# Kernel tuning notes

Measured on AMD Instinct MI355X. Metric: run time of the kernel, lower is better.

The kernel has to match this reference:

```python
import jax, jax.numpy as jnp
import numpy as np

W_PAD = 1  # reflection pad / stencil half-width
CLAMP_MIN = 0.071
EPS = 1e-05


def _laplacian_kernel():
    k = 2 * W_PAD + 1
    ker = -jnp.ones((1, 1, k, k, k), dtype=jnp.float32)
    ker = ker.at[0, 0, W_PAD, W_PAD, W_PAD].set(float(k * k * k - 1))
    return ker  # [O=1, I=1, 3, 3, 3]


def _boundary_weight(pred):
    # pred: [B, L, D, H, W] raw logits
    B, L, D, H, Wd = pred.shape
    ps = jax.nn.softmax(pred, axis=1).astype(jnp.float32)
    # reflect-pad spatial dims by 1, then clamp (matches torch: pad then clamp)
    p = jnp.pad(ps, ((0, 0), (0, 0), (1, 1), (1, 1), (1, 1)), mode='reflect')
    p = jnp.clip(p, CLAMP_MIN)
    # single-channel 3x3x3 stencil applied independently per (batch, label)
    x = p.reshape(B * L, 1, D + 2, H + 2, Wd + 2)
    bt = jax.lax.conv_general_dilated(
        x, _laplacian_kernel(), window_strides=(1, 1, 1), padding='VALID',
        dimension_numbers=('NCDHW', 'OIDHW', 'NCDHW'))
    bt = jnp.abs(bt).reshape(B, L, D, H, Wd)
    bt = jax.lax.stop_gradient(bt)  # torch .detach()
    return 0.5 / (bt + 0.5)


def _dice_bpm(y_pred, y_true, bpm):
    vol_axes = tuple(range(2, y_pred.ndim))  # spatial dims
    top = 2.0 * jnp.sum(y_true * y_pred * bpm, axis=vol_axes)
    bottom = jnp.clip(jnp.sum((y_true + y_pred) * bpm, axis=vol_axes), EPS)
    return -jnp.mean(top / bottom)


def setup_inputs() -> dict:
    key = jax.random.key(0)
    k1, k2 = jax.random.split(key)
    shape = (2, 8, 128, 128, 128)
    pred = jax.random.normal(k1, shape, dtype=jnp.float32)
    target = jax.random.uniform(k2, shape, dtype=jnp.float32)
    return {"pred": pred, "target": target}


def reference(pred, target):
    focal_weight = _boundary_weight(pred)
    return _dice_bpm(pred, target, focal_weight)
```

## Files before the change

### kernel.cpp

```cpp
#include <hip/hip_runtime.h>

constexpr int Dd = 128, Hh = 128, Ww = 128;
constexpr int B_ = 2, L_ = 8;
constexpr int S_SP = Dd * Hh * Ww;
constexpr float CLAMP_MIN = 0.071f;
constexpr float EPS = 1e-5f;

constexpr int TIL = 16;
constexpr int HALO = TIL + 2;
constexpr int DCH = 16;
constexpr int NPOS = HALO * HALO;
constexpr int BLK_PER_B = (Dd / DCH) * (Hh / TIL) * (Ww / TIL);
constexpr int NBLK = B_ * BLK_PER_B;

__device__ __forceinline__ int refl(int x, int n) {
  return x < 0 ? 1 : (x >= n ? n - 2 : x);
}

__global__ __launch_bounds__(256) void fused_kernel(
    const float* __restrict__ pred, const float* __restrict__ tgt,
    float* __restrict__ partial) {
  __shared__ float sps[NPOS][L_];
  __shared__ float red[4][16];

  int blk = blockIdx.x;
  int tw = blk & 7, th = (blk >> 3) & 7, dc = (blk >> 6) & 7, b = blk >> 9;
  int h0 = th * TIL, w0 = tw * TIL, d0 = dc * DCH;
  int tid = threadIdx.x;
  int hl = tid >> 4, wl = tid & 15;
  const float* predb = pred + (size_t)b * L_ * S_SP;

  float s2m[L_], s2c[L_], s2n[L_], ctrc[L_], ctrn[L_];
  float atop[L_], abot[L_];
#pragma unroll
  for (int l = 0; l < L_; ++l) { atop[l] = 0.f; abot[l] = 0.f; }

  for (int pp = -1; pp <= DCH; ++pp) {
    int pd = d0 + pp;
    int rpd = pd < 0 ? 1 : (pd >= Dd ? Dd - 2 : pd);
    __syncthreads();
    for (int pos = tid; pos < NPOS; pos += 256) {
      int i = pos / HALO, j = pos - i * HALO;
      int gh = refl(h0 - 1 + i, Hh);
      int gw = refl(w0 - 1 + j, Ww);
      const float* src = predb + (size_t)rpd * Hh * Ww + gh * Ww + gw;
      float v[L_];
      float m = -1e30f;
#pragma unroll
      for (int l = 0; l < L_; ++l) { v[l] = src[(size_t)l * S_SP]; m = fmaxf(m, v[l]); }
      float s = 0.f;
#pragma unroll
      for (int l = 0; l < L_; ++l) { v[l] = __expf(v[l] - m); s += v[l]; }
      float inv = 1.f / s;
#pragma unroll
      for (int l = 0; l < L_; ++l) v[l] = fmaxf(v[l] * inv, CLAMP_MIN);
      float4* dst = (float4*)&sps[pos][0];
      dst[0] = make_float4(v[0], v[1], v[2], v[3]);
      dst[1] = make_float4(v[4], v[5], v[6], v[7]);
    }
    __syncthreads();
#pragma unroll
    for (int l = 0; l < L_; ++l) s2n[l] = 0.f;
#pragma unroll
    for (int di = 0; di < 3; ++di) {
#pragma unroll
      for (int dj = 0; dj < 3; ++dj) {
        const float4* q = (const float4*)&sps[(hl + di) * HALO + (wl + dj)][0];
        float4 a = q[0], c4 = q[1];
        s2n[0] += a.x;  s2n[1] += a.y;  s2n[2] += a.z;  s2n[3] += a.w;
        s2n[4] += c4.x; s2n[5] += c4.y; s2n[6] += c4.z; s2n[7] += c4.w;
        if (di == 1 && dj == 1) {
          ctrn[0] = a.x;  ctrn[1] = a.y;  ctrn[2] = a.z;  ctrn[3] = a.w;
          ctrn[4] = c4.x; ctrn[5] = c4.y; ctrn[6] = c4.z; ctrn[7] = c4.w;
        }
      }
    }
    if (pp >= 1) {
      int d = pd - 1;
      size_t off0 = (size_t)b * L_ * S_SP + (size_t)d * Hh * Ww + (h0 + hl) * Ww + (w0 + wl);
#pragma unroll
      for (int l = 0; l < L_; ++l) {
        float sum27 = s2m[l] + s2c[l] + s2n[l];
        float bt = fabsf(27.f * ctrc[l] - sum27);
        float bw = 0.5f / (bt + 0.5f);
        size_t off = off0 + (size_t)l * S_SP;
        float p = pred[off];
        float t = tgt[off];
        atop[l] += t * p * bw;
        abot[l] += (t + p) * bw;
      }
    }
#pragma unroll
    for (int l = 0; l < L_; ++l) { s2m[l] = s2c[l]; s2c[l] = s2n[l]; ctrc[l] = ctrn[l]; }
  }

#pragma unroll
  for (int l = 0; l < L_; ++l) {
#pragma unroll
    for (int o = 32; o > 0; o >>= 1) {
      atop[l] += __shfl_down(atop[l], o, 64);
      abot[l] += __shfl_down(abot[l], o, 64);
    }
  }
  int lane = tid & 63, wv = tid >> 6;
  if (lane == 0) {
#pragma unroll
    for (int l = 0; l < L_; ++l) { red[wv][l * 2] = atop[l]; red[wv][l * 2 + 1] = abot[l]; }
  }
  __syncthreads();
  if (tid < 16) {
    float v = red[0][tid] + red[1][tid] + red[2][tid] + red[3][tid];
    partial[blk * 16 + tid] = v;
  }
}

__global__ void finalize_kernel(const float* __restrict__ partial, float* __restrict__ out) {
  __shared__ float rr[16];
  int t = threadIdx.x;
  int p = t >> 4, k = t & 15;
  int b = p >> 3, l = p & 7;
  float top = 0.f, bot = 0.f;
  for (int m = 0; m < BLK_PER_B / 16; ++m) {
    int blk = b * BLK_PER_B + k * (BLK_PER_B / 16) + m;
    top += partial[blk * 16 + l * 2];
    bot += partial[blk * 16 + l * 2 + 1];
  }
#pragma unroll
  for (int o = 8; o > 0; o >>= 1) {
    top += __shfl_down(top, o, 16);
    bot += __shfl_down(bot, o, 16);
  }
  if (k == 0) rr[p] = 2.f * top / fmaxf(bot, EPS);
  __syncthreads();
  if (t == 0) {
    float s = 0.f;
#pragma unroll
    for (int i = 0; i < 16; ++i) s += rr[i];
    out[0] = -s / 16.f;
  }
}

extern "C" void kernel_launch(void* const* d_in, const int* in_sizes, int n_in,
                              void* d_out, int out_size, void* d_ws, size_t ws_size,
                              hipStream_t stream) {
  const float* pred = (const float*)d_in[0];
  const float* tgt  = (const float*)d_in[1];
  float* partial = (float*)d_ws;

  fused_kernel<<<NBLK, 256, 0, stream>>>(pred, tgt, partial);
  finalize_kernel<<<1, 256, 0, stream>>>(partial, (float*)d_out);
}
```

Baseline: 345.6 us.

## Prefetch next depth slice's halo into registers and halve depth chunk

Loads the next depth plane's halo logits into registers while the current plane is processed through softmax and stencil, so global loads overlap with compute and LDS work. The depth chunk per block drops from 16 to 8, doubling the block count for more parallelism at the cost of more redundant halo planes (10 loaded per 8 output instead of 18 per 16). Register pressure rises from holding two extra 8-element prefetch buffers.

```diff
diff --git a/kernel.cpp b/kernel.cpp
--- a/kernel.cpp
+++ b/kernel.cpp
@@ -8,13 +8,40 @@
 
 constexpr int TIL = 16;
 constexpr int HALO = TIL + 2;
-constexpr int DCH = 16;
+constexpr int DCH = 8;
 constexpr int NPOS = HALO * HALO;
-constexpr int BLK_PER_B = (Dd / DCH) * (Hh / TIL) * (Ww / TIL);
+constexpr int NDC = Dd / DCH;
+constexpr int BLK_PER_B = NDC * (Hh / TIL) * (Ww / TIL);
 constexpr int NBLK = B_ * BLK_PER_B;
 
 __device__ __forceinline__ int refl(int x, int n) {
   return x < 0 ? 1 : (x >= n ? n - 2 : x);
+}
+
+__device__ __forceinline__ void halo_load(const float* __restrict__ predb,
+                                          int rpd, int h0, int w0, int pos,
+                                          float v[L_]) {
+  int i = pos / HALO, j = pos - i * HALO;
+  int gh = refl(h0 - 1 + i, Hh);
+  int gw = refl(w0 - 1 + j, Ww);
+  const float* src = predb + (size_t)rpd * Hh * Ww + gh * Ww + gw;
+#pragma unroll
+  for (int l = 0; l < L_; ++l) v[l] = src[(size_t)l * S_SP];
+}
+
+__device__ __forceinline__ void softmax_store(float v[L_], float* dst8) {
+  float m = v[0];
+#pragma unroll
+  for (int l = 1; l < L_; ++l) m = fmaxf(m, v[l]);
+  float s = 0.f;
+#pragma unroll
+  for (int l = 0; l < L_; ++l) { v[l] = __expf(v[l] - m); s += v[l]; }
+  float inv = 1.f / s;
+#pragma unroll
+  for (int l = 0; l < L_; ++l) v[l] = fmaxf(v[l] * inv, CLAMP_MIN);
+  float4* dst = (float4*)dst8;
+  dst[0] = make_float4(v[0], v[1], v[2], v[3]);
+  dst[1] = make_float4(v[4], v[5], v[6], v[7]);
 }
 
 __global__ __launch_bounds__(256) void fused_kernel(
@@ -24,39 +51,35 @@
   __shared__ float red[4][16];
 
   int blk = blockIdx.x;
-  int tw = blk & 7, th = (blk >> 3) & 7, dc = (blk >> 6) & 7, b = blk >> 9;
+  int tw = blk & 7, th = (blk >> 3) & 7, dc = (blk >> 6) & 15, b = blk >> 10;
   int h0 = th * TIL, w0 = tw * TIL, d0 = dc * DCH;
   int tid = threadIdx.x;
   int hl = tid >> 4, wl = tid & 15;
   const float* predb = pred + (size_t)b * L_ * S_SP;
+  const bool has2 = (tid + 256) < NPOS;
 
   float s2m[L_], s2c[L_], s2n[L_], ctrc[L_], ctrn[L_];
   float atop[L_], abot[L_];
 #pragma unroll
   for (int l = 0; l < L_; ++l) { atop[l] = 0.f; abot[l] = 0.f; }
 
+  float v0[L_], v1[L_];
+  {
+    int pd = d0 - 1;
+    int rpd = pd < 0 ? 1 : (pd >= Dd ? Dd - 2 : pd);
+    halo_load(predb, rpd, h0, w0, tid, v0);
+    if (has2) halo_load(predb, rpd, h0, w0, tid + 256, v1);
+  }
+
   for (int pp = -1; pp <= DCH; ++pp) {
-    int pd = d0 + pp;
-    int rpd = pd < 0 ? 1 : (pd >= Dd ? Dd - 2 : pd);
     __syncthreads();
-    for (int pos = tid; pos < NPOS; pos += 256) {
-      int i = pos / HALO, j = pos - i * HALO;
-      int gh = refl(h0 - 1 + i, Hh);
-      int gw = refl(w0 - 1 + j, Ww);
-      const float* src = predb + (size_t)rpd * Hh * Ww + gh * Ww + gw;
-      float v[L_];
-      float m = -1e30f;
-#pragma unroll
-      for (int l = 0; l < L_; ++l) { v[l] = src[(size_t)l * S_SP]; m = fmaxf(m, v[l]); }
-      float s = 0.f;
-#pragma unroll
-      for (int l = 0; l < L_; ++l) { v[l] = __expf(v[l] - m); s += v[l]; }
-      float inv = 1.f / s;
-#pragma unroll
-      for (int l = 0; l < L_; ++l) v[l] = fmaxf(v[l] * inv, CLAMP_MIN);
-      float4* dst = (float4*)&sps[pos][0];
-      dst[0] = make_float4(v[0], v[1], v[2], v[3]);
-      dst[1] = make_float4(v[4], v[5], v[6], v[7]);
+    softmax_store(v0, &sps[tid][0]);
+    if (has2) softmax_store(v1, &sps[tid + 256][0]);
+    if (pp + 1 <= DCH) {
+      int pdn = d0 + pp + 1;
+      int rpdn = pdn < 0 ? 1 : (pdn >= Dd ? Dd - 2 : pdn);
+      halo_load(predb, rpdn, h0, w0, tid, v0);
+      if (has2) halo_load(predb, rpdn, h0, w0, tid + 256, v1);
     }
     __syncthreads();
 #pragma unroll
@@ -76,7 +99,7 @@
       }
     }
     if (pp >= 1) {
-      int d = pd - 1;
+      int d = d0 + pp - 1;
       size_t off0 = (size_t)b * L_ * S_SP + (size_t)d * Hh * Ww + (h0 + hl) * Ww + (w0 + wl);
 #pragma unroll
       for (int l = 0; l < L_; ++l) {
```

Measured after the change: 362.0 us. 1.05x slower.

## Split softmax into fp16 intermediate pass and per-label register stencil kernel

Applied to the files above, without the earlier changes.

Replaces the fused kernel, which recomputed softmax on every halo cell into shared memory, with two passes. The first computes the clamped softmax once per voxel and writes it as fp16. The second runs the 3x3x3 stencil per (batch, label) from registers and wave shuffles, with vectorized loads, then accumulates the dice sums. This removes the halo recomputation and shared-memory traffic but adds a global round trip of about 67MB of fp16 writes and reads, plus reduced precision in the boundary weight.

```diff
diff --git a/kernel.cpp b/kernel.cpp
--- a/kernel.cpp
+++ b/kernel.cpp
@@ -1,4 +1,5 @@
 #include <hip/hip_runtime.h>
+#include <hip/hip_fp16.h>
 
 constexpr int Dd = 128, Hh = 128, Ww = 128;
 constexpr int B_ = 2, L_ = 8;
@@ -6,111 +7,129 @@
 constexpr float CLAMP_MIN = 0.071f;
 constexpr float EPS = 1e-5f;
 
-constexpr int TIL = 16;
-constexpr int HALO = TIL + 2;
-constexpr int DCH = 16;
-constexpr int NPOS = HALO * HALO;
-constexpr int BLK_PER_B = (Dd / DCH) * (Hh / TIL) * (Ww / TIL);
-constexpr int NBLK = B_ * BLK_PER_B;
+constexpr int DCH = 8;
+constexpr int NDC = Dd / DCH;
+constexpr int NHG = Hh / 16;
+constexpr int BLK_PER_P = NDC * NHG;
+constexpr int NBLK2 = B_ * L_ * BLK_PER_P;
 
-__device__ __forceinline__ int refl(int x, int n) {
-  return x < 0 ? 1 : (x >= n ? n - 2 : x);
+__global__ __launch_bounds__(256) void softmax_fp16_kernel(
+    const float* __restrict__ pred, __half* __restrict__ ps) {
+  const int S4 = S_SP / 4;
+  int g = blockIdx.x * 256 + threadIdx.x;
+  int b = g / S4;
+  int s4 = g - b * S4;
+  const float4* in = (const float4*)(pred + (size_t)b * L_ * S_SP) + s4;
+  float v[L_][4];
+#pragma unroll
+  for (int l = 0; l < L_; ++l) {
+    float4 t = in[(size_t)l * S4];
+    v[l][0] = t.x; v[l][1] = t.y; v[l][2] = t.z; v[l][3] = t.w;
+  }
+#pragma unroll
+  for (int c = 0; c < 4; ++c) {
+    float m = v[0][c];
+#pragma unroll
+    for (int l = 1; l < L_; ++l) m = fmaxf(m, v[l][c]);
+    float s = 0.f;
+#pragma unroll
+    for (int l = 0; l < L_; ++l) { v[l][c] = __expf(v[l][c] - m); s += v[l][c]; }
+    float inv = 1.f / s;
+#pragma unroll
+    for (int l = 0; l < L_; ++l) v[l][c] = fmaxf(v[l][c] * inv, CLAMP_MIN);
+  }
+#pragma unroll
+  for (int l = 0; l < L_; ++l) {
+    __half2 h0 = __floats2half2_rn(v[l][0], v[l][1]);
+    __half2 h1 = __floats2half2_rn(v[l][2], v[l][3]);
+    uint2 u;
+    u.x = *(unsigned*)&h0;
+    u.y = *(unsigned*)&h1;
+    *(uint2*)(ps + ((size_t)(b * L_ + l)) * S_SP + (size_t)s4 * 4) = u;
+  }
 }
 
-__global__ __launch_bounds__(256) void fused_kernel(
-    const float* __restrict__ pred, const float* __restrict__ tgt,
-    float* __restrict__ partial) {
-  __shared__ float sps[NPOS][L_];
-  __shared__ float red[4][16];
+__global__ __launch_bounds__(256) void stencil_dice_kernel(
+    const __half* __restrict__ ps, const float* __restrict__ pred,
+    const float* __restrict__ tgt, float* __restrict__ partial) {
+  int blk = blockIdx.x;
+  int dc = blk & 15;
+  int hg = (blk >> 4) & 7;
+  int bl = blk >> 7;
+  int tid = threadIdx.x;
+  int wl = tid & 15, hl = tid >> 4;
+  int h = hg * 16 + hl;
+  int w0 = wl * 8;
+  int d0 = dc * DCH;
+  const __half* P = ps + (size_t)bl * S_SP;
+  int hm = (h == 0) ? 1 : h - 1;
+  int hp = (h == Hh - 1) ? Hh - 2 : h + 1;
 
-  int blk = blockIdx.x;
-  int tw = blk & 7, th = (blk >> 3) & 7, dc = (blk >> 6) & 7, b = blk >> 9;
-  int h0 = th * TIL, w0 = tw * TIL, d0 = dc * DCH;
-  int tid = threadIdx.x;
-  int hl = tid >> 4, wl = tid & 15;
-  const float* predb = pred + (size_t)b * L_ * S_SP;
+  float s2m[8], s2c[8], cprev[8];
+  float top = 0.f, bot = 0.f;
 
-  float s2m[L_], s2c[L_], s2n[L_], ctrc[L_], ctrn[L_];
-  float atop[L_], abot[L_];
+  for (int t = d0 - 1; t <= d0 + DCH; ++t) {
+    int rt = t < 0 ? 1 : (t > Dd - 1 ? Dd - 2 : t);
+    const __half* plane = P + (size_t)rt * Hh * Ww;
+    float s2n[8], ctr[8];
 #pragma unroll
-  for (int l = 0; l < L_; ++l) { atop[l] = 0.f; abot[l] = 0.f; }
-
-  for (int pp = -1; pp <= DCH; ++pp) {
-    int pd = d0 + pp;
-    int rpd = pd < 0 ? 1 : (pd >= Dd ? Dd - 2 : pd);
-    __syncthreads();
-    for (int pos = tid; pos < NPOS; pos += 256) {
-      int i = pos / HALO, j = pos - i * HALO;
-      int gh = refl(h0 - 1 + i, Hh);
-      int gw = refl(w0 - 1 + j, Ww);
-      const float* src = predb + (size_t)rpd * Hh * Ww + gh * Ww + gw;
-      float v[L_];
-      float m = -1e30f;
+    for (int w = 0; w < 8; ++w) s2n[w] = 0.f;
+    int rows[3] = {hm, h, hp};
 #pragma unroll
-      for (int l = 0; l < L_; ++l) { v[l] = src[(size_t)l * S_SP]; m = fmaxf(m, v[l]); }
-      float s = 0.f;
+    for (int ri = 0; ri < 3; ++ri) {
+      uint4 u = *(const uint4*)(plane + rows[ri] * Ww + w0);
+      float f[8];
+      __half2 a;
+      a = *(__half2*)&u.x; { float2 q = __half22float2(a); f[0] = q.x; f[1] = q.y; }
+      a = *(__half2*)&u.y; { float2 q = __half22float2(a); f[2] = q.x; f[3] = q.y; }
+      a = *(__half2*)&u.z; { float2 q = __half22float2(a); f[4] = q.x; f[5] = q.y; }
+      a = *(__half2*)&u.w; { float2 q = __half22float2(a); f[6] = q.x; f[7] = q.y; }
+      float lf = __shfl_up(f[7], 1, 64);
+      if (wl == 0) lf = f[1];
+      float rg = __shfl_down(f[0], 1, 64);
+      if (wl == 15) rg = f[6];
+      s2n[0] += lf + f[0] + f[1];
 #pragma unroll
-      for (int l = 0; l < L_; ++l) { v[l] = __expf(v[l] - m); s += v[l]; }
-      float inv = 1.f / s;
+      for (int w = 1; w < 7; ++w) s2n[w] += f[w - 1] + f[w] + f[w + 1];
+      s2n[7] += f[6] + f[7] + rg;
+      if (ri == 1) {
 #pragma unroll
-      for (int l = 0; l < L_; ++l) v[l] = fmaxf(v[l] * inv, CLAMP_MIN);
-      float4* dst = (float4*)&sps[pos][0];
-      dst[0] = make_float4(v[0], v[1], v[2], v[3]);
-      dst[1] = make_float4(v[4], v[5], v[6], v[7]);
-    }
-    __syncthreads();
-#pragma unroll
-    for (int l = 0; l < L_; ++l) s2n[l] = 0.f;
-#pragma unroll
-    for (int di = 0; di < 3; ++di) {
-#pragma unroll
-      for (int dj = 0; dj < 3; ++dj) {
-        const float4* q = (const float4*)&sps[(hl + di) * HALO + (wl + dj)][0];
-        float4 a = q[0], c4 = q[1];
-        s2n[0] += a.x;  s2n[1] += a.y;  s2n[2] += a.z;  s2n[3] += a.w;
-        s2n[4] += c4.x; s2n[5] += c4.y; s2n[6] += c4.z; s2n[7] += c4.w;
-        if (di == 1 && dj == 1) {
-          ctrn[0] = a.x;  ctrn[1] = a.y;  ctrn[2] = a.z;  ctrn[3] = a.w;
-          ctrn[4] = c4.x; ctrn[5] = c4.y; ctrn[6] = c4.z; ctrn[7] = c4.w;
-        }
+        for (int w = 0; w < 8; ++w) ctr[w] = f[w];
       }
     }
-    if (pp >= 1) {
-      int d = pd - 1;
-      size_t off0 = (size_t)b * L_ * S_SP + (size_t)d * Hh * Ww + (h0 + hl) * Ww + (w0 + wl);
+    if (t >= d0 + 1) {
+      int d = t - 1;
+      size_t off = (size_t)bl * S_SP + (size_t)d * Hh * Ww + (size_t)h * Ww + w0;
+      float4 p0 = *(const float4*)(pred + off);
+      float4 p1 = *(const float4*)(pred + off + 4);
+      float4 t0 = *(const float4*)(tgt + off);
+      float4 t1 = *(const float4*)(tgt + off + 4);
+      float pv[8] = {p0.x, p0.y, p0.z, p0.w, p1.x, p1.y, p1.z, p1.w};
+      float tv[8] = {t0.x, t0.y, t0.z, t0.w, t1.x, t1.y, t1.z, t1.w};
 #pragma unroll
-      for (int l = 0; l < L_; ++l) {
-        float sum27 = s2m[l] + s2c[l] + s2n[l];
-        float bt = fabsf(27.f * ctrc[l] - sum27);
+      for (int w = 0; w < 8; ++w) {
+        float bt = fabsf(27.f * cprev[w] - (s2m[w] + s2c[w] + s2n[w]));
         float bw = 0.5f / (bt + 0.5f);
-        size_t off = off0 + (size_t)l * S_SP;
-        float p = pred[off];
-        float t = tgt[off];
-        atop[l] += t * p * bw;
-        abot[l] += (t + p) * bw;
+        top += tv[w] * pv[w] * bw;
+        bot += (tv[w] + pv[w]) * bw;
       }
     }
 #pragma unroll
-    for (int l = 0; l < L_; ++l) { s2m[l] = s2c[l]; s2c[l] = s2n[l]; ctrc[l] = ctrn[l]; }
+    for (int w = 0; w < 8; ++w) { s2m[w] = s2c[w]; s2c[w] = s2n[w]; cprev[w] = ctr[w]; }
   }
 
 #pragma unroll
-  for (int l = 0; l < L_; ++l) {
-#pragma unroll
-    for (int o = 32; o > 0; o >>= 1) {
-      atop[l] += __shfl_down(atop[l], o, 64);
-      abot[l] += __shfl_down(abot[l], o, 64);
-    }
+  for (int o = 32; o > 0; o >>= 1) {
+    top += __shfl_down(top, o, 64);
+    bot += __shfl_down(bot, o, 64);
   }
+  __shared__ float st[4], sb[4];
   int lane = tid & 63, wv = tid >> 6;
-  if (lane == 0) {
-#pragma unroll
-    for (int l = 0; l < L_; ++l) { red[wv][l * 2] = atop[l]; red[wv][l * 2 + 1] = abot[l]; }
-  }
+  if (lane == 0) { st[wv] = top; sb[wv] = bot; }
   __syncthreads();
-  if (tid < 16) {
-    float v = red[0][tid] + red[1][tid] + red[2][tid] + red[3][tid];
-    partial[blk * 16 + tid] = v;
+  if (tid == 0) {
+    partial[blk * 2 + 0] = st[0] + st[1] + st[2] + st[3];
+    partial[blk * 2 + 1] = sb[0] + sb[1] + sb[2] + sb[3];
   }
 }
 
@@ -118,12 +137,11 @@
   __shared__ float rr[16];
   int t = threadIdx.x;
   int p = t >> 4, k = t & 15;
-  int b = p >> 3, l = p & 7;
   float top = 0.f, bot = 0.f;
-  for (int m = 0; m < BLK_PER_B / 16; ++m) {
-    int blk = b * BLK_PER_B + k * (BLK_PER_B / 16) + m;
-    top += partial[blk * 16 + l * 2];
-    bot += partial[blk * 16 + l * 2 + 1];
+  for (int m = 0; m < BLK_PER_P / 16; ++m) {
+    int blk = p * BLK_PER_P + k * (BLK_PER_P / 16) + m;
+    top += partial[blk * 2 + 0];
+    bot += partial[blk * 2 + 1];
   }
 #pragma unroll
   for (int o = 8; o > 0; o >>= 1) {
@@ -145,8 +163,11 @@
                               hipStream_t stream) {
   const float* pred = (const float*)d_in[0];
   const float* tgt  = (const float*)d_in[1];
-  float* partial = (float*)d_ws;
+  __half* ps = (__half*)d_ws;
+  float* partial = (float*)((char*)d_ws + (size_t)B_ * L_ * S_SP * sizeof(__half));
 
-  fused_kernel<<<NBLK, 256, 0, stream>>>(pred, tgt, partial);
+  int g1 = (B_ * (S_SP / 4)) / 256;
+  softmax_fp16_kernel<<<g1, 256, 0, stream>>>(pred, ps);
+  stencil_dice_kernel<<<NBLK2, 256, 0, stream>>>(ps, pred, tgt, partial);
   finalize_kernel<<<1, 256, 0, stream>>>(partial, (float*)d_out);
 }
```

Result: faster. 315.3 us (-8.8%).

## Replace LDS halo tiles with row-per-wave softmax recompute and lane shuffles

Applied to the files above, without the earlier changes.

Each wave now covers a full 128-wide W row, with two voxels per lane. W-direction neighbours come from lane shuffles, and the H neighbours are handled by recomputing the softmax for three rows per thread. This removes the shared-memory halo tile and its per-plane barriers. The raw pred value for the center row is kept in registers and reused in the dice accumulation instead of being reloaded. In exchange, exp/softmax work roughly triples in H, and pred row reads become redundant, relying on cache.

```diff
diff --git a/kernel.cpp b/kernel.cpp
--- a/kernel.cpp
+++ b/kernel.cpp
@@ -6,106 +6,125 @@
 constexpr float CLAMP_MIN = 0.071f;
 constexpr float EPS = 1e-5f;
 
-constexpr int TIL = 16;
-constexpr int HALO = TIL + 2;
-constexpr int DCH = 16;
-constexpr int NPOS = HALO * HALO;
-constexpr int BLK_PER_B = (Dd / DCH) * (Hh / TIL) * (Ww / TIL);
+constexpr int DCH = 8;
+constexpr int NDC = Dd / DCH;
+constexpr int HG = 4;
+constexpr int NHG = Hh / HG;
+constexpr int BLK_PER_B = NHG * NDC;
 constexpr int NBLK = B_ * BLK_PER_B;
 
-__device__ __forceinline__ int refl(int x, int n) {
-  return x < 0 ? 1 : (x >= n ? n - 2 : x);
-}
-
-__global__ __launch_bounds__(256) void fused_kernel(
+__global__ __launch_bounds__(256) void fused_all_kernel(
     const float* __restrict__ pred, const float* __restrict__ tgt,
     float* __restrict__ partial) {
-  __shared__ float sps[NPOS][L_];
-  __shared__ float red[4][16];
+  int blk = blockIdx.x;
+  int dc = blk & 15;
+  int hg = (blk >> 4) & 31;
+  int b  = blk >> 9;
+  int tid = threadIdx.x;
+  int wl = tid & 63;
+  int hl = tid >> 6;
+  int h = hg * HG + hl;
+  int w0 = wl * 2;
+  int d0 = dc * DCH;
+  const float* pb = pred + (size_t)b * L_ * S_SP;
+  const float* tb = tgt  + (size_t)b * L_ * S_SP;
+  int hm = (h == 0) ? 1 : h - 1;
+  int hp = (h == Hh - 1) ? Hh - 2 : h + 1;
+  int rows[3] = {hm, h, hp};
 
-  int blk = blockIdx.x;
-  int tw = blk & 7, th = (blk >> 3) & 7, dc = (blk >> 6) & 7, b = blk >> 9;
-  int h0 = th * TIL, w0 = tw * TIL, d0 = dc * DCH;
-  int tid = threadIdx.x;
-  int hl = tid >> 4, wl = tid & 15;
-  const float* predb = pred + (size_t)b * L_ * S_SP;
+  float s2m[L_][2], s2c[L_][2], cprev[L_][2], rawm[L_][2];
+  float top[L_], bot[L_];
+#pragma unroll
+  for (int l = 0; l < L_; ++l) { top[l] = 0.f; bot[l] = 0.f; }
 
-  float s2m[L_], s2c[L_], s2n[L_], ctrc[L_], ctrn[L_];
-  float atop[L_], abot[L_];
+  for (int t = d0 - 1; t <= d0 + DCH; ++t) {
+    int rt = t < 0 ? 1 : (t > Dd - 1 ? Dd - 2 : t);
+    const float* plane = pb + (size_t)rt * Hh * Ww;
+    float s2n[L_][2], ctr[L_][2], rawn[L_][2];
 #pragma unroll
-  for (int l = 0; l < L_; ++l) { atop[l] = 0.f; abot[l] = 0.f; }
+    for (int l = 0; l < L_; ++l) { s2n[l][0] = 0.f; s2n[l][1] = 0.f; }
 
-  for (int pp = -1; pp <= DCH; ++pp) {
-    int pd = d0 + pp;
-    int rpd = pd < 0 ? 1 : (pd >= Dd ? Dd - 2 : pd);
-    __syncthreads();
-    for (int pos = tid; pos < NPOS; pos += 256) {
-      int i = pos / HALO, j = pos - i * HALO;
-      int gh = refl(h0 - 1 + i, Hh);
-      int gw = refl(w0 - 1 + j, Ww);
-      const float* src = predb + (size_t)rpd * Hh * Ww + gh * Ww + gw;
-      float v[L_];
-      float m = -1e30f;
 #pragma unroll
-      for (int l = 0; l < L_; ++l) { v[l] = src[(size_t)l * S_SP]; m = fmaxf(m, v[l]); }
-      float s = 0.f;
+    for (int ri = 0; ri < 3; ++ri) {
+      const float* rp = plane + rows[ri] * Ww + w0;
+      float f0[L_], f1[L_];
 #pragma unroll
-      for (int l = 0; l < L_; ++l) { v[l] = __expf(v[l] - m); s += v[l]; }
-      float inv = 1.f / s;
+      for (int l = 0; l < L_; ++l) {
+        float2 v = *(const float2*)(rp + (size_t)l * S_SP);
+        f0[l] = v.x; f1[l] = v.y;
+      }
+      float p0[L_], p1[L_];
+      {
+        float m0 = f0[0], m1 = f1[0];
 #pragma unroll
-      for (int l = 0; l < L_; ++l) v[l] = fmaxf(v[l] * inv, CLAMP_MIN);
-      float4* dst = (float4*)&sps[pos][0];
-      dst[0] = make_float4(v[0], v[1], v[2], v[3]);
-      dst[1] = make_float4(v[4], v[5], v[6], v[7]);
-    }
-    __syncthreads();
+        for (int l = 1; l < L_; ++l) { m0 = fmaxf(m0, f0[l]); m1 = fmaxf(m1, f1[l]); }
+        float s0 = 0.f, s1 = 0.f;
 #pragma unroll
-    for (int l = 0; l < L_; ++l) s2n[l] = 0.f;
+        for (int l = 0; l < L_; ++l) {
+          p0[l] = __expf(f0[l] - m0); s0 += p0[l];
+          p1[l] = __expf(f1[l] - m1); s1 += p1[l];
+        }
+        float i0 = 1.f / s0, i1 = 1.f / s1;
 #pragma unroll
-    for (int di = 0; di < 3; ++di) {
-#pragma unroll
-      for (int dj = 0; dj < 3; ++dj) {
-        const float4* q = (const float4*)&sps[(hl + di) * HALO + (wl + dj)][0];
-        float4 a = q[0], c4 = q[1];
-        s2n[0] += a.x;  s2n[1] += a.y;  s2n[2] += a.z;  s2n[3] += a.w;
-        s2n[4] += c4.x; s2n[5] += c4.y; s2n[6] += c4.z; s2n[7] += c4.w;
-        if (di == 1 && dj == 1) {
-          ctrn[0] = a.x;  ctrn[1] = a.y;  ctrn[2] = a.z;  ctrn[3] = a.w;
-          ctrn[4] = c4.x; ctrn[5] = c4.y; ctrn[6] = c4.z; ctrn[7] = c4.w;
+        for (int l = 0; l < L_; ++l) {
+          p0[l] = fmaxf(p0[l] * i0, CLAMP_MIN);
+          p1[l] = fmaxf(p1[l] * i1, CLAMP_MIN);
         }
       }
-    }
-    if (pp >= 1) {
-      int d = pd - 1;
-      size_t off0 = (size_t)b * L_ * S_SP + (size_t)d * Hh * Ww + (h0 + hl) * Ww + (w0 + wl);
+      if (ri == 1) {
+#pragma unroll
+        for (int l = 0; l < L_; ++l) {
+          rawn[l][0] = f0[l]; rawn[l][1] = f1[l];
+          ctr[l][0] = p0[l];  ctr[l][1] = p1[l];
+        }
+      }
 #pragma unroll
       for (int l = 0; l < L_; ++l) {
-        float sum27 = s2m[l] + s2c[l] + s2n[l];
-        float bt = fabsf(27.f * ctrc[l] - sum27);
-        float bw = 0.5f / (bt + 0.5f);
-        size_t off = off0 + (size_t)l * S_SP;
-        float p = pred[off];
-        float t = tgt[off];
-        atop[l] += t * p * bw;
-        abot[l] += (t + p) * bw;
+        float lf = __shfl_up(p1[l], 1, 64);
+        if (wl == 0) lf = p1[l];
+        float rg = __shfl_down(p0[l], 1, 64);
+        if (wl == 63) rg = p0[l];
+        s2n[l][0] += lf + p0[l] + p1[l];
+        s2n[l][1] += p0[l] + p1[l] + rg;
+      }
+    }
+
+    if (t >= d0 + 1) {
+      int d = t - 1;
+      const float* trow = tb + (size_t)d * Hh * Ww + (size_t)h * Ww + w0;
+#pragma unroll
+      for (int l = 0; l < L_; ++l) {
+        float2 tv = *(const float2*)(trow + (size_t)l * S_SP);
+        float bt0 = fabsf(27.f * cprev[l][0] - (s2m[l][0] + s2c[l][0] + s2n[l][0]));
+        float bt1 = fabsf(27.f * cprev[l][1] - (s2m[l][1] + s2c[l][1] + s2n[l][1]));
+        float bw0 = 0.5f / (bt0 + 0.5f);
+        float bw1 = 0.5f / (bt1 + 0.5f);
+        top[l] += tv.x * rawm[l][0] * bw0 + tv.y * rawm[l][1] * bw1;
+        bot[l] += (tv.x + rawm[l][0]) * bw0 + (tv.y + rawm[l][1]) * bw1;
       }
     }
 #pragma unroll
-    for (int l = 0; l < L_; ++l) { s2m[l] = s2c[l]; s2c[l] = s2n[l]; ctrc[l] = ctrn[l]; }
+    for (int l = 0; l < L_; ++l) {
+      s2m[l][0] = s2c[l][0]; s2m[l][1] = s2c[l][1];
+      s2c[l][0] = s2n[l][0]; s2c[l][1] = s2n[l][1];
+      cprev[l][0] = ctr[l][0]; cprev[l][1] = ctr[l][1];
+      rawm[l][0] = rawn[l][0]; rawm[l][1] = rawn[l][1];
+    }
   }
 
 #pragma unroll
   for (int l = 0; l < L_; ++l) {
 #pragma unroll
     for (int o = 32; o > 0; o >>= 1) {
-      atop[l] += __shfl_down(atop[l], o, 64);
-      abot[l] += __shfl_down(abot[l], o, 64);
+      top[l] += __shfl_down(top[l], o, 64);
+      bot[l] += __shfl_down(bot[l], o, 64);
     }
   }
+  __shared__ float red[4][16];
   int lane = tid & 63, wv = tid >> 6;
   if (lane == 0) {
 #pragma unroll
-    for (int l = 0; l < L_; ++l) { red[wv][l * 2] = atop[l]; red[wv][l * 2 + 1] = abot[l]; }
+    for (int l = 0; l < L_; ++l) { red[wv][l * 2] = top[l]; red[wv][l * 2 + 1] = bot[l]; }
   }
   __syncthreads();
   if (tid < 16) {
@@ -147,6 +166,6 @@
   const float* tgt  = (const float*)d_in[1];
   float* partial = (float*)d_ws;
 
-  fused_kernel<<<NBLK, 256, 0, stream>>>(pred, tgt, partial);
+  fused_all_kernel<<<NBLK, 256, 0, stream>>>(pred, tgt, partial);
   finalize_kernel<<<1, 256, 0, stream>>>(partial, (float*)d_out);
 }
```

Result: faster. 315.5 us (-8.7%).
